# Optimization experiments

Measured on AMD Instinct MI355X. Metric: run time of the kernel, lower is better.

The kernel has to match this reference:

```python
import jax, jax.numpy as jnp
import numpy as np

NUM_CLASSES = 8
EPS = 1e-4  # variance epsilon from the original module
MARGIN = 1.0  # __init__ arg; unused in the forward math


def setup_inputs() -> dict:
    key = jax.random.key(0)
    kf, kl = jax.random.split(key)
    features = jax.random.normal(kf, (65536, 2, 256), dtype=jnp.float32)
    labels = jax.random.randint(kl, (65536,), 0, NUM_CLASSES)
    return {"features": features, "labels": labels}


def _loss(features, labels):
    B, V, D = features.shape
    # Views of each sample are stacked into the sample's class group
    X = features.reshape(B * V, D)              # [N, D]
    lab = jnp.repeat(labels, V)                 # [N]
    onehot = (lab[:, None] == jnp.arange(NUM_CLASSES)[None, :]).astype(X.dtype)  # [N, C]

    counts = onehot.sum(axis=0)                 # [C] per-class row counts (all > 1 by construction)
    sums = onehot.T @ X                         # [C, D]
    means = sums / counts[:, None]              # [C, D]
    e2 = onehot.T @ (X * X)                     # [C, D] per-class sum of squares
    # unbiased per-feature variance (torch.var default, ddof=1)
    var = (e2 - counts[:, None] * means * means) / (counts[:, None] - 1.0)
    std = jnp.sqrt(var + EPS)
    std_loss = jnp.sum(jnp.mean(jax.nn.relu(1.0 - std), axis=1))  # sum over classes of mean over features

    # Per-class covariance: cov_c = (X_c - mu_c)^T (X_c - mu_c) / (n_c - 1)
    #                             = (sum_c x x^T - n_c mu mu^T) / (n_c - 1)
    S = jnp.einsum('nc,nd,ne->cde', onehot, X, X)  # [C, D, D]
    cov = (S - counts[:, None, None] * means[:, :, None] * means[:, None, :]) / (
        counts[:, None, None] - 1.0)
    diag = jnp.diagonal(cov, axis1=1, axis2=2)      # [C, D]
    offdiag_sq = jnp.sum(cov * cov, axis=(1, 2)) - jnp.sum(diag * diag, axis=1)
    cov_loss = jnp.sum(offdiag_sq / D)

    return std_loss + cov_loss


def reference(features, labels):
    return _loss(features, labels)
```

## Files before the change

kernel.cpp:

```cpp
#include <hip/hip_runtime.h>
#include <stdint.h>


#define NCLS  8
#define D     256
#define CHUNK 1024
#define SEG   256
#define EPSF  1e-4f
#define TMAX  144

typedef __bf16 bf16x8 __attribute__((ext_vector_type(8)));
typedef float  f32x4  __attribute__((ext_vector_type(4)));

__device__ __forceinline__ unsigned short f2bf(float f) {
    unsigned int x = __float_as_uint(f);
    x += 0x7fffu + ((x >> 16) & 1u);
    return (unsigned short)(x >> 16);
}

__global__ void k_hist(const int* __restrict__ labels, int nlab, int vfac,
                       int* __restrict__ counts) {
    __shared__ int lc[NCLS];
    int t = threadIdx.x;
    if (t < NCLS) lc[t] = 0;
    __syncthreads();
    for (int i = blockIdx.x * blockDim.x + t; i < nlab; i += gridDim.x * blockDim.x)
        atomicAdd(&lc[labels[i] & 7], vfac);
    __syncthreads();
    if (t < NCLS && lc[t]) atomicAdd(&counts[t], lc[t]);
}

__global__ void k_offsets(const int* __restrict__ counts,
                          int* __restrict__ offsets, int* __restrict__ cursor) {
    if (threadIdx.x == 0) {
        int acc = 0;
        for (int c = 0; c < NCLS; ++c) { offsets[c] = acc; cursor[c] = acc; acc += counts[c]; }
    }
}

__global__ __launch_bounds__(256) void k_idx(
    const int* __restrict__ labels, int nrows, int vfac,
    int* __restrict__ cursor, int* __restrict__ idx)
{
    __shared__ int lcnt[NCLS], lbase[NCLS];
    int t = threadIdx.x;
    int row = blockIdx.x * SEG + t;
    if (t < NCLS) lcnt[t] = 0;
    __syncthreads();
    int c = 0, rk = 0;
    bool ok = (row < nrows);
    if (ok) {
        c = labels[row / vfac] & 7;
        rk = atomicAdd(&lcnt[c], 1);
    }
    __syncthreads();
    if (t < NCLS) lbase[t] = lcnt[t] ? atomicAdd(&cursor[t], lcnt[t]) : 0;
    __syncthreads();
    if (ok) idx[lbase[c] + rk] = row;
}

__global__ __launch_bounds__(512) void k_gram_g(
    const float* __restrict__ X, const int* __restrict__ idx,
    const int* __restrict__ counts, const int* __restrict__ offsets,
    float* __restrict__ part, float* __restrict__ csums)
{
    __shared__ __align__(16) unsigned char lds[64 * 256 * 2];

    int t = threadIdx.x;
    int lane = t & 63;
    int w = t >> 6;
    int wrow = w >> 1;
    int wcol = w & 1;
    int kblk = t & 15;
    int cblk = t >> 4;

    int nch[NCLS], ofch[NCLS];
    int T = 0;
    for (int c = 0; c < NCLS; ++c) {
        int n = counts[c];
        nch[c] = (n + CHUNK - 1) / CHUNK;
        ofch[c] = T;
        T += nch[c];
    }

    const f32x4 zf = {0.f, 0.f, 0.f, 0.f};

    for (int wk = blockIdx.x; wk < 2 * T; wk += gridDim.x) {
        int item = wk >> 1;
        int half = wk & 1;
        int c = 0;
        while (c < NCLS - 1 && item >= ofch[c + 1]) ++c;
        int chunk = item - ofch[c];
        int base = offsets[c] + chunk * CHUNK;
        int rows = min(CHUNK, counts[c] - chunk * CHUNK);
        int ntiles = (rows + 63) >> 6;

        f32x4 acc[4][4];
        #pragma unroll
        for (int i = 0; i < 4; ++i)
            #pragma unroll
            for (int j = 0; j < 4; ++j)
                #pragma unroll
                for (int r = 0; r < 4; ++r) acc[i][j][r] = 0.f;
        float sumv[8];
        #pragma unroll
        for (int q = 0; q < 8; ++q) sumv[q] = 0.f;

        for (int kt = 0; kt < ntiles; ++kt) {
            uint4 R[4];
            #pragma unroll
            for (int j = 0; j < 4; ++j) {
                int r = kt * 64 + kblk * 4 + j;
                f32x4 fa, fb;
                if (r < rows) {
                    int rid = idx[base + r];
                    const float* rp = X + ((size_t)rid << 8) + cblk * 8;
                    fa = *(const f32x4*)rp;
                    fb = *(const f32x4*)(rp + 4);
                } else { fa = zf; fb = zf; }
                #pragma unroll
                for (int q = 0; q < 4; ++q) { sumv[q] += fa[q]; sumv[4 + q] += fb[q]; }
                unsigned int w0 = (unsigned int)f2bf(fa[0]) | ((unsigned int)f2bf(fa[1]) << 16);
                unsigned int w1 = (unsigned int)f2bf(fa[2]) | ((unsigned int)f2bf(fa[3]) << 16);
                unsigned int w2 = (unsigned int)f2bf(fb[0]) | ((unsigned int)f2bf(fb[1]) << 16);
                unsigned int w3 = (unsigned int)f2bf(fb[2]) | ((unsigned int)f2bf(fb[3]) << 16);
                R[j] = make_uint4(w0, w1, w2, w3);
            }
            __syncthreads();
            #pragma unroll
            for (int cc = 0; cc < 8; ++cc) {
                int wd = cc >> 1;
                int sh = (cc & 1) * 16;
                unsigned int e0 = (((const unsigned int*)&R[0])[wd] >> sh) & 0xffffu;
                unsigned int e1 = (((const unsigned int*)&R[1])[wd] >> sh) & 0xffffu;
                unsigned int e2 = (((const unsigned int*)&R[2])[wd] >> sh) & 0xffffu;
                unsigned int e3 = (((const unsigned int*)&R[3])[wd] >> sh) & 0xffffu;
                int ccol = cblk * 8 + cc;
                int byt = ccol * 128 + ((kblk * 8) ^ (cc << 4));
                *(uint2*)(lds + byt) = make_uint2(e0 | (e1 << 16), e2 | (e3 << 16));
            }
            __syncthreads();
            #pragma unroll
            for (int ks = 0; ks < 2; ++ks) {
                int kb2 = ks * 64 + ((lane >> 4) << 4);
                int swz = (lane & 7) << 4;
                bf16x8 bfr[4];
                #pragma unroll
                for (int tj = 0; tj < 4; ++tj) {
                    int ccol = half * 128 + wcol * 64 + tj * 16 + (lane & 15);
                    bfr[tj] = __builtin_bit_cast(bf16x8,
                        *(const uint4*)(lds + ccol * 128 + (kb2 ^ swz)));
                }
                #pragma unroll
                for (int ti = 0; ti < 4; ++ti) {
                    int ccol = wrow * 64 + ti * 16 + (lane & 15);
                    bf16x8 af = __builtin_bit_cast(bf16x8,
                        *(const uint4*)(lds + ccol * 128 + (kb2 ^ swz)));
                    #pragma unroll
                    for (int tj = 0; tj < 4; ++tj)
                        acc[ti][tj] = __builtin_amdgcn_mfma_f32_16x16x32_bf16(
                            af, bfr[tj], acc[ti][tj], 0, 0, 0);
                }
            }
        }

        float* dst = part + (size_t)item * (D * D);
        #pragma unroll
        for (int ti = 0; ti < 4; ++ti) {
            int row0 = wrow * 64 + ti * 16 + ((lane >> 4) << 2);
            #pragma unroll
            for (int tj = 0; tj < 4; ++tj) {
                int col = half * 128 + wcol * 64 + tj * 16 + (lane & 15);
                #pragma unroll
                for (int r = 0; r < 4; ++r)
                    dst[(row0 + r) * D + col] = acc[ti][tj][r];
            }
        }

        #pragma unroll
        for (int s = 1; s < 16; s <<= 1)
            #pragma unroll
            for (int q = 0; q < 8; ++q)
                sumv[q] += __shfl_xor(sumv[q], s, 64);
        if (half == 0 && (t & 15) == 0) {
            float* cs = csums + (size_t)item * D + cblk * 8;
            #pragma unroll
            for (int q = 0; q < 8; ++q) cs[q] = sumv[q];
        }
        __syncthreads();
    }
}

__global__ __launch_bounds__(256) void k_gsum(
    const float* __restrict__ csums, const int* __restrict__ counts,
    float* __restrict__ gsums)
{
    int c = blockIdx.x;
    int i = threadIdx.x;
    int of = 0;
    for (int cc = 0; cc < c; ++cc) of += (counts[cc] + CHUNK - 1) / CHUNK;
    int nc = (counts[c] + CHUNK - 1) / CHUNK;
    float s = 0.f;
    for (int q = 0; q < nc; ++q) s += csums[(size_t)(of + q) * D + i];
    gsums[c * D + i] = s;
}

__global__ __launch_bounds__(256) void k_loss(
    const float* __restrict__ part, const float* __restrict__ gsums,
    const int* __restrict__ counts, float* __restrict__ out)
{
    __shared__ float red[256];
    int t = threadIdx.x;
    int nch[NCLS], ofch[NCLS];
    int T = 0;
    for (int c = 0; c < NCLS; ++c) {
        int n = counts[c];
        nch[c] = (n + CHUNK - 1) / CHUNK;
        ofch[c] = T;
        T += nch[c];
    }
    float local = 0.f;
    const int total = NCLS * D * D;
    for (int idx = blockIdx.x * blockDim.x + t; idx < total; idx += gridDim.x * blockDim.x) {
        int c = idx >> 16;
        int ij = idx & 0xffff;
        int i = ij >> 8, j = ij & 255;
        const float* p = part + (size_t)ofch[c] * (D * D) + ij;
        float s = 0.f;
        for (int q = 0; q < nch[c]; ++q) s += p[(size_t)q * (D * D)];
        float n  = (float)counts[c];
        float mi = gsums[c * D + i] / n;
        float mj = gsums[c * D + j] / n;
        float cov = (s - n * mi * mj) / (n - 1.f);
        float contrib;
        if (i == j) {
            float sd = sqrtf(cov + EPSF);
            contrib = fmaxf(1.f - sd, 0.f) * (1.f / (float)D);
        } else {
            contrib = cov * cov * (1.f / (float)D);
        }
        local += contrib;
    }
    red[t] = local;
    __syncthreads();
    for (int s = 128; s > 0; s >>= 1) {
        if (t < s) red[t] += red[t + s];
        __syncthreads();
    }
    if (t == 0) atomicAdd(out, red[0]);
}

extern "C" void kernel_launch(void* const* d_in, const int* in_sizes, int n_in,
                              void* d_out, int out_size, void* d_ws, size_t ws_size,
                              hipStream_t stream)
{
    const float* X      = (const float*)d_in[0];
    const int*   labels = (const int*)d_in[1];
    int nfeat = in_sizes[0];
    int nlab  = in_sizes[1];
    int nrows = nfeat / D;
    int vfac  = nrows / nlab;

    char* ws = (char*)d_ws;
    size_t off_idx   = 0;
    size_t sz_idx    = (size_t)nrows * 4;
    size_t off_part  = (off_idx + sz_idx + 255) & ~(size_t)255;
    size_t sz_part   = (size_t)TMAX * D * D * 4;
    size_t off_cs    = (off_part + sz_part + 255) & ~(size_t)255;
    size_t sz_cs     = (size_t)TMAX * D * 4;
    size_t off_gs    = (off_cs + sz_cs + 255) & ~(size_t)255;
    size_t sz_gs     = (size_t)NCLS * D * 4;
    size_t off_cnt   = (off_gs + sz_gs + 255) & ~(size_t)255;
    size_t off_ofs   = off_cnt + 64;
    size_t off_cur   = off_ofs + 64;

    int*   idx     = (int*)(ws + off_idx);
    float* part    = (float*)(ws + off_part);
    float* csums   = (float*)(ws + off_cs);
    float* gsums   = (float*)(ws + off_gs);
    int*   counts  = (int*)(ws + off_cnt);
    int*   offsets = (int*)(ws + off_ofs);
    int*   cursor  = (int*)(ws + off_cur);

    hipMemsetAsync(counts, 0, 64, stream);
    hipMemsetAsync(d_out, 0, (size_t)out_size * sizeof(float), stream);

    k_hist<<<64, 256, 0, stream>>>(labels, nlab, vfac, counts);
    k_offsets<<<1, 64, 0, stream>>>(counts, offsets, cursor);
    k_idx<<<(nrows + SEG - 1) / SEG, SEG, 0, stream>>>(labels, nrows, vfac, cursor, idx);
    k_gram_g<<<2 * TMAX, 512, 0, stream>>>(X, idx, counts, offsets, part, csums);
    k_gsum<<<NCLS, 256, 0, stream>>>(csums, counts, gsums);
    k_loss<<<512, 256, 0, stream>>>(part, gsums, counts, (float*)d_out);
}
```

Before: 134.0 us.

## Exploit Gram symmetry with three 128x128 blocks and store bf16 partials

The Gram matrix is split into three 128x128 quadrants (two diagonal blocks plus one off-diagonal block counted twice) instead of two 256x128 halves, so the redundant lower-left block is never computed. Partial sums are now written in bf16 instead of fp32, which halves partial-buffer traffic. Chunk size drops to 512 rows with 256-thread blocks, giving more independent work items. In exchange, precision of the partial sums is reduced, which risks error in the covariance loss. There is also more gather traffic for the off-diagonal item, which loads both column halves.

```diff
diff --git a/kernel.cpp b/kernel.cpp
--- a/kernel.cpp
+++ b/kernel.cpp
@@ -4,10 +4,11 @@
 
 #define NCLS  8
 #define D     256
-#define CHUNK 1024
+#define CHUNK 512
 #define SEG   256
 #define EPSF  1e-4f
-#define TMAX  144
+#define TMAX  264
+#define QLEN  16384
 
 typedef __bf16 bf16x8 __attribute__((ext_vector_type(8)));
 typedef float  f32x4  __attribute__((ext_vector_type(4)));
@@ -16,6 +17,31 @@
     unsigned int x = __float_as_uint(f);
     x += 0x7fffu + ((x >> 16) & 1u);
     return (unsigned short)(x >> 16);
+}
+__device__ __forceinline__ float bf2f(unsigned short u) {
+    return __uint_as_float(((unsigned int)u) << 16);
+}
+__device__ __forceinline__ uint4 pack8(const f32x4& a, const f32x4& b) {
+    return make_uint4(
+        (unsigned int)f2bf(a[0]) | ((unsigned int)f2bf(a[1]) << 16),
+        (unsigned int)f2bf(a[2]) | ((unsigned int)f2bf(a[3]) << 16),
+        (unsigned int)f2bf(b[0]) | ((unsigned int)f2bf(b[1]) << 16),
+        (unsigned int)f2bf(b[2]) | ((unsigned int)f2bf(b[3]) << 16));
+}
+__device__ __forceinline__ void st_tile(unsigned char* lds, const uint4* R,
+                                        int kblk, int cblkg) {
+    #pragma unroll
+    for (int cc = 0; cc < 8; ++cc) {
+        int wd = cc >> 1;
+        int sh = (cc & 1) * 16;
+        unsigned int e0 = (((const unsigned int*)&R[0])[wd] >> sh) & 0xffffu;
+        unsigned int e1 = (((const unsigned int*)&R[1])[wd] >> sh) & 0xffffu;
+        unsigned int e2 = (((const unsigned int*)&R[2])[wd] >> sh) & 0xffffu;
+        unsigned int e3 = (((const unsigned int*)&R[3])[wd] >> sh) & 0xffffu;
+        int ccol = cblkg * 8 + cc;
+        int byt = ccol * 128 + ((kblk * 8) ^ (cc << 4));
+        *(uint2*)(lds + byt) = make_uint2(e0 | (e1 << 16), e2 | (e3 << 16));
+    }
 }
 
 __global__ void k_hist(const int* __restrict__ labels, int nlab, int vfac,
@@ -59,20 +85,19 @@
     if (ok) idx[lbase[c] + rk] = row;
 }
 
-__global__ __launch_bounds__(512) void k_gram_g(
+__global__ __launch_bounds__(256) void k_gram_g(
     const float* __restrict__ X, const int* __restrict__ idx,
     const int* __restrict__ counts, const int* __restrict__ offsets,
-    float* __restrict__ part, float* __restrict__ csums)
+    unsigned short* __restrict__ part, float* __restrict__ csums)
 {
     __shared__ __align__(16) unsigned char lds[64 * 256 * 2];
 
     int t = threadIdx.x;
     int lane = t & 63;
     int w = t >> 6;
-    int wrow = w >> 1;
-    int wcol = w & 1;
+    int wrow = w >> 1, wcol = w & 1;
     int kblk = t & 15;
-    int cblk = t >> 4;
+    int cblk0 = t >> 4;
 
     int nch[NCLS], ofch[NCLS];
     int T = 0;
@@ -85,9 +110,9 @@
 
     const f32x4 zf = {0.f, 0.f, 0.f, 0.f};
 
-    for (int wk = blockIdx.x; wk < 2 * T; wk += gridDim.x) {
-        int item = wk >> 1;
-        int half = wk & 1;
+    for (int wk = blockIdx.x; wk < 3 * T; wk += gridDim.x) {
+        int item = wk / 3;
+        int q = wk - item * 3;
         int c = 0;
         while (c < NCLS - 1 && item >= ofch[c + 1]) ++c;
         int chunk = item - ofch[c];
@@ -95,6 +120,10 @@
         int rows = min(CHUNK, counts[c] - chunk * CHUNK);
         int ntiles = (rows + 63) >> 6;
 
+        int colb = (q == 1) ? 128 : 0;
+        bool two = (q == 2);
+        int bbase = two ? 128 : 0;
+
         f32x4 acc[4][4];
         #pragma unroll
         for (int i = 0; i < 4; ++i)
@@ -104,41 +133,42 @@
                 for (int r = 0; r < 4; ++r) acc[i][j][r] = 0.f;
         float sumv[8];
         #pragma unroll
-        for (int q = 0; q < 8; ++q) sumv[q] = 0.f;
+        for (int e = 0; e < 8; ++e) sumv[e] = 0.f;
 
         for (int kt = 0; kt < ntiles; ++kt) {
-            uint4 R[4];
+            int rid[4];
             #pragma unroll
             for (int j = 0; j < 4; ++j) {
                 int r = kt * 64 + kblk * 4 + j;
-                f32x4 fa, fb;
-                if (r < rows) {
-                    int rid = idx[base + r];
-                    const float* rp = X + ((size_t)rid << 8) + cblk * 8;
-                    fa = *(const f32x4*)rp;
-                    fb = *(const f32x4*)(rp + 4);
-                } else { fa = zf; fb = zf; }
-                #pragma unroll
-                for (int q = 0; q < 4; ++q) { sumv[q] += fa[q]; sumv[4 + q] += fb[q]; }
-                unsigned int w0 = (unsigned int)f2bf(fa[0]) | ((unsigned int)f2bf(fa[1]) << 16);
-                unsigned int w1 = (unsigned int)f2bf(fa[2]) | ((unsigned int)f2bf(fa[3]) << 16);
-                unsigned int w2 = (unsigned int)f2bf(fb[0]) | ((unsigned int)f2bf(fb[1]) << 16);
-                unsigned int w3 = (unsigned int)f2bf(fb[2]) | ((unsigned int)f2bf(fb[3]) << 16);
-                R[j] = make_uint4(w0, w1, w2, w3);
+                rid[j] = idx[base + min(r, rows - 1)];
+            }
+            uint4 R0[4];
+            #pragma unroll
+            for (int j = 0; j < 4; ++j) {
+                int r = kt * 64 + kblk * 4 + j;
+                const float* rp = X + ((size_t)rid[j] << 8) + colb + cblk0 * 8;
+                f32x4 a = *(const f32x4*)rp;
+                f32x4 b = *(const f32x4*)(rp + 4);
+                if (r >= rows) { a = zf; b = zf; }
+                #pragma unroll
+                for (int e = 0; e < 4; ++e) { sumv[e] += a[e]; sumv[4 + e] += b[e]; }
+                R0[j] = pack8(a, b);
+            }
+            uint4 R1[4];
+            if (two) {
+                #pragma unroll
+                for (int j = 0; j < 4; ++j) {
+                    int r = kt * 64 + kblk * 4 + j;
+                    const float* rp = X + ((size_t)rid[j] << 8) + 128 + cblk0 * 8;
+                    f32x4 a = *(const f32x4*)rp;
+                    f32x4 b = *(const f32x4*)(rp + 4);
+                    if (r >= rows) { a = zf; b = zf; }
+                    R1[j] = pack8(a, b);
+                }
             }
             __syncthreads();
-            #pragma unroll
-            for (int cc = 0; cc < 8; ++cc) {
-                int wd = cc >> 1;
-                int sh = (cc & 1) * 16;
-                unsigned int e0 = (((const unsigned int*)&R[0])[wd] >> sh) & 0xffffu;
-                unsigned int e1 = (((const unsigned int*)&R[1])[wd] >> sh) & 0xffffu;
-                unsigned int e2 = (((const unsigned int*)&R[2])[wd] >> sh) & 0xffffu;
-                unsigned int e3 = (((const unsigned int*)&R[3])[wd] >> sh) & 0xffffu;
-                int ccol = cblk * 8 + cc;
-                int byt = ccol * 128 + ((kblk * 8) ^ (cc << 4));
-                *(uint2*)(lds + byt) = make_uint2(e0 | (e1 << 16), e2 | (e3 << 16));
-            }
+            st_tile(lds, R0, kblk, cblk0);
+            if (two) st_tile(lds, R1, kblk, cblk0 + 16);
             __syncthreads();
             #pragma unroll
             for (int ks = 0; ks < 2; ++ks) {
@@ -147,7 +177,7 @@
                 bf16x8 bfr[4];
                 #pragma unroll
                 for (int tj = 0; tj < 4; ++tj) {
-                    int ccol = half * 128 + wcol * 64 + tj * 16 + (lane & 15);
+                    int ccol = bbase + wcol * 64 + tj * 16 + (lane & 15);
                     bfr[tj] = __builtin_bit_cast(bf16x8,
                         *(const uint4*)(lds + ccol * 128 + (kb2 ^ swz)));
                 }
@@ -164,28 +194,28 @@
             }
         }
 
-        float* dst = part + (size_t)item * (D * D);
+        unsigned short* dst = part + (size_t)wk * QLEN;
         #pragma unroll
         for (int ti = 0; ti < 4; ++ti) {
             int row0 = wrow * 64 + ti * 16 + ((lane >> 4) << 2);
             #pragma unroll
             for (int tj = 0; tj < 4; ++tj) {
-                int col = half * 128 + wcol * 64 + tj * 16 + (lane & 15);
+                int col = wcol * 64 + tj * 16 + (lane & 15);
                 #pragma unroll
                 for (int r = 0; r < 4; ++r)
-                    dst[(row0 + r) * D + col] = acc[ti][tj][r];
+                    dst[(row0 + r) * 128 + col] = f2bf(acc[ti][tj][r]);
             }
         }
 
         #pragma unroll
         for (int s = 1; s < 16; s <<= 1)
             #pragma unroll
-            for (int q = 0; q < 8; ++q)
-                sumv[q] += __shfl_xor(sumv[q], s, 64);
-        if (half == 0 && (t & 15) == 0) {
-            float* cs = csums + (size_t)item * D + cblk * 8;
-            #pragma unroll
-            for (int q = 0; q < 8; ++q) cs[q] = sumv[q];
+            for (int e = 0; e < 8; ++e)
+                sumv[e] += __shfl_xor(sumv[e], s, 64);
+        if (q < 2 && (t & 15) == 0) {
+            float* cs = csums + (size_t)item * D + colb + cblk0 * 8;
+            #pragma unroll
+            for (int e = 0; e < 8; ++e) cs[e] = sumv[e];
         }
         __syncthreads();
     }
@@ -206,7 +236,7 @@
 }
 
 __global__ __launch_bounds__(256) void k_loss(
-    const float* __restrict__ part, const float* __restrict__ gsums,
+    const unsigned short* __restrict__ part, const float* __restrict__ gsums,
     const int* __restrict__ counts, float* __restrict__ out)
 {
     __shared__ float red[256];
@@ -220,20 +250,26 @@
         T += nch[c];
     }
     float local = 0.f;
-    const int total = NCLS * D * D;
+    const int total = NCLS * 3 * QLEN;
     for (int idx = blockIdx.x * blockDim.x + t; idx < total; idx += gridDim.x * blockDim.x) {
-        int c = idx >> 16;
-        int ij = idx & 0xffff;
-        int i = ij >> 8, j = ij & 255;
-        const float* p = part + (size_t)ofch[c] * (D * D) + ij;
+        int c = idx / (3 * QLEN);
+        int rem = idx - c * (3 * QLEN);
+        int q = rem >> 14;
+        int ij = rem & (QLEN - 1);
+        int il = ij >> 7, jl = ij & 127;
+        int gi = il + ((q == 1) ? 128 : 0);
+        int gj = jl + ((q == 0) ? 0 : 128);
+        const unsigned short* p = part + ((size_t)(ofch[c] * 3 + q)) * QLEN + ij;
         float s = 0.f;
-        for (int q = 0; q < nch[c]; ++q) s += p[(size_t)q * (D * D)];
+        for (int k = 0; k < nch[c]; ++k) s += bf2f(p[(size_t)k * 3 * QLEN]);
         float n  = (float)counts[c];
-        float mi = gsums[c * D + i] / n;
-        float mj = gsums[c * D + j] / n;
+        float mi = gsums[c * D + gi] / n;
+        float mj = gsums[c * D + gj] / n;
         float cov = (s - n * mi * mj) / (n - 1.f);
         float contrib;
-        if (i == j) {
+        if (q == 2) {
+            contrib = 2.f * cov * cov * (1.f / (float)D);
+        } else if (il == jl) {
             float sd = sqrtf(cov + EPSF);
             contrib = fmaxf(1.f - sd, 0.f) * (1.f / (float)D);
         } else {
@@ -265,7 +301,7 @@
     size_t off_idx   = 0;
     size_t sz_idx    = (size_t)nrows * 4;
     size_t off_part  = (off_idx + sz_idx + 255) & ~(size_t)255;
-    size_t sz_part   = (size_t)TMAX * D * D * 4;
+    size_t sz_part   = (size_t)3 * TMAX * QLEN * 2;
     size_t off_cs    = (off_part + sz_part + 255) & ~(size_t)255;
     size_t sz_cs     = (size_t)TMAX * D * 4;
     size_t off_gs    = (off_cs + sz_cs + 255) & ~(size_t)255;
@@ -274,13 +310,13 @@
     size_t off_ofs   = off_cnt + 64;
     size_t off_cur   = off_ofs + 64;
 
-    int*   idx     = (int*)(ws + off_idx);
-    float* part    = (float*)(ws + off_part);
-    float* csums   = (float*)(ws + off_cs);
-    float* gsums   = (float*)(ws + off_gs);
-    int*   counts  = (int*)(ws + off_cnt);
-    int*   offsets = (int*)(ws + off_ofs);
-    int*   cursor  = (int*)(ws + off_cur);
+    int*            idx     = (int*)(ws + off_idx);
+    unsigned short* part    = (unsigned short*)(ws + off_part);
+    float*          csums   = (float*)(ws + off_cs);
+    float*          gsums   = (float*)(ws + off_gs);
+    int*            counts  = (int*)(ws + off_cnt);
+    int*            offsets = (int*)(ws + off_ofs);
+    int*            cursor  = (int*)(ws + off_cur);
 
     hipMemsetAsync(counts, 0, 64, stream);
     hipMemsetAsync(d_out, 0, (size_t)out_size * sizeof(float), stream);
@@ -288,7 +324,7 @@
     k_hist<<<64, 256, 0, stream>>>(labels, nlab, vfac, counts);
     k_offsets<<<1, 64, 0, stream>>>(counts, offsets, cursor);
     k_idx<<<(nrows + SEG - 1) / SEG, SEG, 0, stream>>>(labels, nrows, vfac, cursor, idx);
-    k_gram_g<<<2 * TMAX, 512, 0, stream>>>(X, idx, counts, offsets, part, csums);
+    k_gram_g<<<3 * TMAX, 256, 0, stream>>>(X, idx, counts, offsets, part, csums);
     k_gsum<<<NCLS, 256, 0, stream>>>(csums, counts, gsums);
     k_loss<<<512, 256, 0, stream>>>(part, gsums, counts, (float*)d_out);
 }
```

Result: no change. 134.6 us (+0.4%).
